# Kernel tuning notes

Hardware: AMD Instinct MI355X
Metric: run time of the kernel (lower is better)

The kernel has to match this reference:

```python
import jax, jax.numpy as jnp
import numpy as np

B, H, W = 4, 496, 496
M = 8  # max vertices of a quad-quad convex intersection


def _corners(boxes):
    # boxes [..., 7] = (x, y, z, dx, dy, dz, heading) -> CCW BEV corners [..., 4, 2]
    x, y, dx, dy, r = boxes[..., 0], boxes[..., 1], boxes[..., 3], boxes[..., 4], boxes[..., 6]
    lx = jnp.array([0.5, -0.5, -0.5, 0.5], dtype=boxes.dtype) * dx[..., None]
    ly = jnp.array([0.5, 0.5, -0.5, -0.5], dtype=boxes.dtype) * dy[..., None]
    c, s = jnp.cos(r)[..., None], jnp.sin(r)[..., None]
    cx = x[..., None] + c * lx - s * ly
    cy = y[..., None] + s * lx + c * ly
    return jnp.stack([cx, cy], axis=-1)


def _clip(poly, cnt, a, b):
    # Clip padded CCW polygon (poly [M,2], cnt valid verts) by halfplane left of edge a->b.
    idx = jnp.arange(M)
    valid = idx < cnt
    nidx = jnp.where(idx + 1 >= cnt, 0, idx + 1)
    cur, nxt = poly, poly[nidx]
    ex, ey = b[0] - a[0], b[1] - a[1]
    dc = ex * (cur[:, 1] - a[1]) - ey * (cur[:, 0] - a[0])  # signed dist of cur
    dn = ex * (nxt[:, 1] - a[1]) - ey * (nxt[:, 0] - a[0])
    inc, inn = dc >= 0, dn >= 0
    keep = inc & valid                      # emit cur if inside
    crs = (inc != inn) & valid              # emit edge/line intersection if crossing
    den = dc - dn
    t = dc / jnp.where(jnp.abs(den) < 1e-9, 1.0, den)
    ip = cur + t[:, None] * (nxt - cur)
    c = keep.astype(jnp.int32) + crs.astype(jnp.int32)
    offs = jnp.cumsum(c) - c                # exclusive prefix sum -> output slots
    out = jnp.zeros_like(poly)
    out = out.at[jnp.where(keep, offs, M)].set(cur, mode='drop')
    out = out.at[jnp.where(crs, offs + keep.astype(jnp.int32), M)].set(ip, mode='drop')
    return out, jnp.sum(c)


def _inter_area(ca, cb):
    # Intersection area of two CCW quads (each [4,2]) via Sutherland-Hodgman.
    poly = jnp.zeros((M, 2), ca.dtype).at[:4].set(ca)
    cnt = jnp.int32(4)
    for i in range(4):
        poly, cnt = _clip(poly, cnt, cb[i], cb[(i + 1) % 4])
    idx = jnp.arange(M)
    valid = idx < cnt
    nidx = jnp.where(idx + 1 >= cnt, 0, idx + 1)
    nxt = poly[nidx]
    cr = poly[:, 0] * nxt[:, 1] - nxt[:, 0] * poly[:, 1]  # shoelace terms
    return 0.5 * jnp.abs(jnp.sum(jnp.where(valid, cr, 0.0)))


def _iou3d_aligned(boxes_a, boxes_b):
    # Element-wise (aligned) 3D oriented-box IoU. boxes [N,7] -> iou [N].
    inter_bev = jax.vmap(_inter_area)(_corners(boxes_a), _corners(boxes_b))
    za0, za1 = boxes_a[:, 2] - 0.5 * boxes_a[:, 5], boxes_a[:, 2] + 0.5 * boxes_a[:, 5]
    zb0, zb1 = boxes_b[:, 2] - 0.5 * boxes_b[:, 5], boxes_b[:, 2] + 0.5 * boxes_b[:, 5]
    zo = jnp.maximum(jnp.minimum(za1, zb1) - jnp.maximum(za0, zb0), 0.0)
    inter_vol = inter_bev * zo
    vol_a = boxes_a[:, 3] * boxes_a[:, 4] * boxes_a[:, 5]
    vol_b = boxes_b[:, 3] * boxes_b[:, 4] * boxes_b[:, 5]
    return inter_vol / (vol_a + vol_b - inter_vol + 1e-7)


def setup_inputs() -> dict:
    key = jax.random.key(0)
    kc, kd, kr, kn, km, kp, ki = jax.random.split(key, 7)
    center = jax.random.normal(kc, (B, H, W, 3), dtype=jnp.float32) * 2.0
    dims = jax.random.uniform(kd, (B, H, W, 3), minval=0.5, maxval=3.0, dtype=jnp.float32)
    heading = jax.random.uniform(kr, (B, H, W, 1), minval=-np.pi, maxval=np.pi, dtype=jnp.float32)
    box_gt = jnp.concatenate([center, dims, heading], axis=-1)  # [B,H,W,7]
    pred = box_gt + jax.random.normal(kn, box_gt.shape, dtype=jnp.float32) * 0.1
    pred = pred.at[..., 3:6].set(jnp.maximum(pred[..., 3:6], 0.2))  # keep dims positive
    box_pred = jnp.transpose(pred, (0, 3, 1, 2))  # [B,7,H,W]
    mask = jax.random.randint(km, (B, H, W), 0, 2, dtype=jnp.int32)
    iou_pred = jax.random.normal(kp, (B, H, W), dtype=jnp.float32) * 0.5
    ind = jax.random.randint(ki, (B, 128), 0, H * W, dtype=jnp.int32)  # unused by the layer
    return {"iou_pred": iou_pred, "mask": mask, "ind": ind, "box_pred": box_pred, "box_gt": box_gt}


def reference(iou_pred, mask, ind, box_pred, box_gt):
    pred = jnp.transpose(box_pred, (0, 2, 3, 1)).reshape(-1, 7)  # [N,7]
    gt = box_gt.reshape(-1, 7)
    target = 2.0 * _iou3d_aligned(pred, gt) - 1.0               # [N]
    m = mask.astype(jnp.float32).reshape(-1)
    loss = jnp.sum(m * jnp.abs(iou_pred.reshape(-1) - target))
    return loss / (jnp.sum(m) + 1e-4)
```

## Files before the change

### kernel.cpp

```cpp
#include <hip/hip_runtime.h>
#include <math.h>

#define B_   4
#define H_   496
#define W_   496
#define HW_  (H_ * W_)
#define N_   (B_ * HW_)
#define TPB  256
#define NPT  2
#define EPB  (TPB * NPT)
#define NBLK (N_ / EPB)

static_assert(N_ % EPB == 0, "no tail");

__device__ __forceinline__ float edge_delta(float xk, float yk,
                                            float dx, float dy,
                                            float rdx, float rdy,
                                            float hx, float hy) {
    float t0 = 0.f, t1 = 1.f, tl;
    tl = __builtin_amdgcn_fmed3f((hy - yk) * rdy, 0.f, 1.f);
    t0 = fmaxf(t0, (dy < 0.f) ? tl : 0.f);
    t1 = fminf(t1, (dy > 0.f) ? tl : 1.f);
    tl = __builtin_amdgcn_fmed3f(-(xk + hx) * rdx, 0.f, 1.f);
    t0 = fmaxf(t0, (dx > 0.f) ? tl : 0.f);
    t1 = fminf(t1, (dx < 0.f) ? tl : 1.f);
    tl = __builtin_amdgcn_fmed3f(-(yk + hy) * rdy, 0.f, 1.f);
    t0 = fmaxf(t0, (dy > 0.f) ? tl : 0.f);
    t1 = fminf(t1, (dy < 0.f) ? tl : 1.f);
    tl = __builtin_amdgcn_fmed3f((hx - xk) * rdx, 0.f, 1.f);
    t0 = fmaxf(t0, (dx < 0.f) ? tl : 0.f);
    t1 = fminf(t1, (dx > 0.f) ? tl : 1.f);
    return fmaxf(t1 - t0, 0.f);
}

__device__ __forceinline__ void iou_elem(
    int n, const float* __restrict__ iou_pred, const int* __restrict__ mask,
    const float* __restrict__ box_pred, const float* __restrict__ sg7,
    float& num, float& den)
{
    const int b  = n / HW_;
    const int hw = n - b * HW_;

    const float* bp = box_pred + (size_t)b * 7 * HW_ + hw;
    const float pax = bp[0];
    const float pay = bp[1 * HW_];
    const float paz = bp[2 * HW_];
    const float pdx = bp[3 * HW_];
    const float pdy = bp[4 * HW_];
    const float pdz = bp[5 * HW_];
    const float pr  = bp[6 * HW_];

    const float gax = sg7[0], gay = sg7[1], gaz = sg7[2];
    const float gdx = sg7[3], gdy = sg7[4], gdz = sg7[5], gr = sg7[6];

    float sp, cp; __sincosf(pr, &sp, &cp);
    float sg, cg; __sincosf(gr, &sg, &cg);
    const float cth = fmaf(cp, cg,  sp * sg);
    const float sth = fmaf(sp, cg, -cp * sg);
    const float wx = pax - gax, wy = pay - gay;
    const float cx = fmaf(cg, wx,  sg * wy);
    const float cy = fmaf(cg, wy, -sg * wx);

    const float phx = 0.5f * pdx, phy = 0.5f * pdy;
    const float ghx = 0.5f * gdx, ghy = 0.5f * gdy;

    const float a1 = cth * phx, b1 = sth * phx;
    const float a2 = sth * phy, b2 = cth * phy;
    const float e1 = a1 - a2, e2 = a1 + a2;
    const float f1 = b1 + b2, f2 = b1 - b2;
    const float px0 = cx + e1, py0 = cy + f1;
    const float px1 = cx - e2, py1 = cy - f2;
    const float px2 = cx - e1, py2 = cy - f1;
    const float px3 = cx + e2, py3 = cy + f2;

    const float ta1 = a1 + a1, tb1 = b1 + b1;
    const float ta2 = a2 + a2, tb2 = b2 + b2;
    const float ra1 = __builtin_amdgcn_rcpf(ta1);
    const float rb1 = __builtin_amdgcn_rcpf(tb1);
    const float ra2 = __builtin_amdgcn_rcpf(ta2);
    const float rb2 = __builtin_amdgcn_rcpf(tb2);

    float inter;
    {
        const float d0 = edge_delta(px0, py0, -ta1, -tb1, -ra1, -rb1, ghx, ghy);
        const float d1 = edge_delta(px1, py1,  ta2, -tb2,  ra2, -rb2, ghx, ghy);
        const float d2 = edge_delta(px2, py2,  ta1,  tb1,  ra1,  rb1, ghx, ghy);
        const float d3 = edge_delta(px3, py3, -ta2,  tb2, -ra2,  rb2, ghx, ghy);
        inter =        d0 * fmaf(a1, py0, -b1 * px0);
        inter = fmaf(  d1, -fmaf(b2, px1,  a2 * py1), inter);
        inter = fmaf(  d2,  fmaf(b1, px2, -a1 * py2), inter);
        inter = fmaf(  d3,  fmaf(b2, px3,  a2 * py3), inter);
    }

    {
        const float A  = cth * ghx, Dv = sth * ghx;
        const float Bq = sth * ghy, Ev = cth * ghy;
        const float Cc = fmaf(cth, cx,  sth * cy);
        const float Gf = fmaf(sth, cx, -cth * cy);
        const float g1 = A + Bq,  g2 = A - Bq;
        const float h1 = Ev - Dv, h2 = Ev + Dv;
        const float u0 =  g1 - Cc, v0 =  h1 + Gf;
        const float u1 = -g2 - Cc, v1 =  h2 + Gf;
        const float u2 = -g1 - Cc, v2 = -h1 + Gf;
        const float u3 =  g2 - Cc, v3 = -h2 + Gf;

        const float tA = A + A,  tD = Dv + Dv;
        const float tB = Bq + Bq, tE = Ev + Ev;
        const float rA = __builtin_amdgcn_rcpf(tA);
        const float rD = __builtin_amdgcn_rcpf(tD);
        const float rB = __builtin_amdgcn_rcpf(tB);
        const float rE = __builtin_amdgcn_rcpf(tE);

        float sq;
        sq  = edge_delta(u0, v0, -tA,  tD, -rA,  rD, phx, phy);
        sq += edge_delta(u1, v1, -tB, -tE, -rB, -rE, phx, phy);
        sq += edge_delta(u2, v2,  tA, -tD,  rA, -rD, phx, phy);
        sq += edge_delta(u3, v3,  tB,  tE,  rB,  rE, phx, phy);
        inter = fmaf(ghx * ghy, sq, inter);
    }

    const float za0 = paz - 0.5f * pdz, za1 = paz + 0.5f * pdz;
    const float zb0 = gaz - 0.5f * gdz, zb1 = gaz + 0.5f * gdz;
    const float zo  = fmaxf(fminf(za1, zb1) - fmaxf(za0, zb0), 0.f);
    const float iv  = inter * zo;
    const float va  = pdx * pdy * pdz;
    const float vb  = gdx * gdy * gdz;
    const float iou = iv / (va + vb - iv + 1e-7f);
    const float target = 2.f * iou - 1.f;

    const float m = (float)mask[n];
    num += m * fabsf(iou_pred[n] - target);
    den += m;
}

__global__ __launch_bounds__(TPB) void iou_main(
    const float* __restrict__ iou_pred,
    const int*   __restrict__ mask,
    const float* __restrict__ box_pred,
    const float* __restrict__ box_gt,
    float2* __restrict__ ws)
{
    __shared__ float sgt[EPB * 7];
    __shared__ float rn[4], rd[4];

    const int tid  = threadIdx.x;
    const int base = blockIdx.x * EPB;

    {
        const float4* g4 = (const float4*)(box_gt + (size_t)base * 7);
        float4* s4 = (float4*)sgt;
#pragma unroll
        for (int it = 0; it < 3; ++it)
            s4[tid + it * TPB] = g4[tid + it * TPB];
        const int idx = tid + 3 * TPB;
        if (idx < (EPB * 7) / 4) s4[idx] = g4[idx];
    }
    __syncthreads();

    float num = 0.f, den = 0.f;
#pragma unroll
    for (int e = 0; e < NPT; ++e) {
        const int n = base + e * TPB + tid;
        iou_elem(n, iou_pred, mask, box_pred, sgt + (e * TPB + tid) * 7, num, den);
    }

#pragma unroll
    for (int off = 32; off > 0; off >>= 1) {
        num += __shfl_down(num, off);
        den += __shfl_down(den, off);
    }
    if ((tid & 63) == 0) { rn[tid >> 6] = num; rd[tid >> 6] = den; }
    __syncthreads();
    if (tid == 0)
        ws[blockIdx.x] = make_float2(rn[0] + rn[1] + rn[2] + rn[3],
                                     rd[0] + rd[1] + rd[2] + rd[3]);
}

__global__ __launch_bounds__(TPB) void iou_fin(const float2* __restrict__ ws,
                                               float* __restrict__ out) {
    __shared__ float rn[4], rd[4];
    float sn = 0.f, sd = 0.f;
    for (int i = threadIdx.x; i < NBLK; i += TPB) {
        const float2 v = ws[i];
        sn += v.x;
        sd += v.y;
    }
#pragma unroll
    for (int off = 32; off > 0; off >>= 1) {
        sn += __shfl_down(sn, off);
        sd += __shfl_down(sd, off);
    }
    const int tid = threadIdx.x;
    if ((tid & 63) == 0) { rn[tid >> 6] = sn; rd[tid >> 6] = sd; }
    __syncthreads();
    if (tid == 0)
        out[0] = (rn[0] + rn[1] + rn[2] + rn[3]) /
                 (rd[0] + rd[1] + rd[2] + rd[3] + 1e-4f);
}

extern "C" void kernel_launch(void* const* d_in, const int* in_sizes, int n_in,
                              void* d_out, int out_size, void* d_ws, size_t ws_size,
                              hipStream_t stream) {
    const float* iou_pred = (const float*)d_in[0];
    const int*   mask     = (const int*)  d_in[1];
    const float* box_pred = (const float*)d_in[3];
    const float* box_gt   = (const float*)d_in[4];
    float*  out = (float*)d_out;
    float2* ws  = (float2*)d_ws;

    iou_main<<<NBLK, TPB, 0, stream>>>(iou_pred, mask, box_pred, box_gt, ws);
    iou_fin<<<1, TPB, 0, stream>>>(ws, out);
}
```

Baseline: 106.1 us.

## Load four contiguous elements per thread with float4 vectors, drop LDS staging

```diff
diff --git a/kernel.cpp b/kernel.cpp
--- a/kernel.cpp
+++ b/kernel.cpp
@@ -7,11 +7,15 @@
 #define HW_  (H_ * W_)
 #define N_   (B_ * HW_)
 #define TPB  256
-#define NPT  2
+#define NPT  4
 #define EPB  (TPB * NPT)
 #define NBLK (N_ / EPB)
 
 static_assert(N_ % EPB == 0, "no tail");
+static_assert(HW_ % NPT == 0, "thread quad must not straddle batch b");
+
+union F4 { float4 v; float a[4]; };
+union I4 { int4 v; int a[4]; };
 
 __device__ __forceinline__ float edge_delta(float xk, float yk,
                                             float dx, float dy,
@@ -34,25 +38,10 @@
 }
 
 __device__ __forceinline__ void iou_elem(
-    int n, const float* __restrict__ iou_pred, const int* __restrict__ mask,
-    const float* __restrict__ box_pred, const float* __restrict__ sg7,
-    float& num, float& den)
+    float pax, float pay, float paz, float pdx, float pdy, float pdz, float pr,
+    float gax, float gay, float gaz, float gdx, float gdy, float gdz, float gr,
+    float ip, float m, float& num, float& den)
 {
-    const int b  = n / HW_;
-    const int hw = n - b * HW_;
-
-    const float* bp = box_pred + (size_t)b * 7 * HW_ + hw;
-    const float pax = bp[0];
-    const float pay = bp[1 * HW_];
-    const float paz = bp[2 * HW_];
-    const float pdx = bp[3 * HW_];
-    const float pdy = bp[4 * HW_];
-    const float pdz = bp[5 * HW_];
-    const float pr  = bp[6 * HW_];
-
-    const float gax = sg7[0], gay = sg7[1], gaz = sg7[2];
-    const float gdx = sg7[3], gdy = sg7[4], gdz = sg7[5], gr = sg7[6];
-
     float sp, cp; __sincosf(pr, &sp, &cp);
     float sg, cg; __sincosf(gr, &sg, &cg);
     const float cth = fmaf(cp, cg,  sp * sg);
@@ -104,7 +93,7 @@
         const float u2 = -g1 - Cc, v2 = -h1 + Gf;
         const float u3 =  g2 - Cc, v3 = -h2 + Gf;
 
-        const float tA = A + A,  tD = Dv + Dv;
+        const float tA = A + A,   tD = Dv + Dv;
         const float tB = Bq + Bq, tE = Ev + Ev;
         const float rA = __builtin_amdgcn_rcpf(tA);
         const float rD = __builtin_amdgcn_rcpf(tD);
@@ -125,11 +114,10 @@
     const float iv  = inter * zo;
     const float va  = pdx * pdy * pdz;
     const float vb  = gdx * gdy * gdz;
-    const float iou = iv / (va + vb - iv + 1e-7f);
+    const float iou = __fdividef(iv, va + vb - iv + 1e-7f);
     const float target = 2.f * iou - 1.f;
 
-    const float m = (float)mask[n];
-    num += m * fabsf(iou_pred[n] - target);
+    num = fmaf(m, fabsf(ip - target), num);
     den += m;
 }
 
@@ -140,28 +128,37 @@
     const float* __restrict__ box_gt,
     float2* __restrict__ ws)
 {
-    __shared__ float sgt[EPB * 7];
     __shared__ float rn[4], rd[4];
 
-    const int tid  = threadIdx.x;
-    const int base = blockIdx.x * EPB;
-
+    const int tid = threadIdx.x;
+    const int n0  = (blockIdx.x * TPB + tid) * NPT;
+    const int b   = n0 / HW_;
+    const int hw  = n0 - b * HW_;
+
+    const float* bp = box_pred + (size_t)b * 7 * HW_ + hw;
+    F4 pc[7];
+#pragma unroll
+    for (int c = 0; c < 7; ++c)
+        pc[c].v = *(const float4*)(bp + (size_t)c * HW_);
+
+    float gtv[28];
     {
-        const float4* g4 = (const float4*)(box_gt + (size_t)base * 7);
-        float4* s4 = (float4*)sgt;
-#pragma unroll
-        for (int it = 0; it < 3; ++it)
-            s4[tid + it * TPB] = g4[tid + it * TPB];
-        const int idx = tid + 3 * TPB;
-        if (idx < (EPB * 7) / 4) s4[idx] = g4[idx];
-    }
-    __syncthreads();
+        const float4* g4 = (const float4*)(box_gt + (size_t)n0 * 7);
+#pragma unroll
+        for (int j = 0; j < 7; ++j)
+            *(float4*)(gtv + 4 * j) = g4[j];
+    }
+    F4 ip4; ip4.v = *(const float4*)(iou_pred + n0);
+    I4 mk4; mk4.v = *(const int4*)(mask + n0);
 
     float num = 0.f, den = 0.f;
 #pragma unroll
     for (int e = 0; e < NPT; ++e) {
-        const int n = base + e * TPB + tid;
-        iou_elem(n, iou_pred, mask, box_pred, sgt + (e * TPB + tid) * 7, num, den);
+        const float* g = gtv + 7 * e;
+        iou_elem(pc[0].a[e], pc[1].a[e], pc[2].a[e],
+                 pc[3].a[e], pc[4].a[e], pc[5].a[e], pc[6].a[e],
+                 g[0], g[1], g[2], g[3], g[4], g[5], g[6],
+                 ip4.a[e], (float)mk4.a[e], num, den);
     }
 
 #pragma unroll
```

Result: no change. 105.8 us (-0.2%).
